# Optimization experiments

Hardware: AMD Instinct MI355X
Metric: run time of the kernel (lower is better)

The kernel has to match this reference:

```python
import jax, jax.numpy as jnp
import numpy as np

EPS = 1e-08

def setup_inputs() -> dict:
    key = jax.random.key(0)
    ks = jax.random.split(key, 5)
    B, T, D, L = 8, 4096, 1024, 24
    data = jax.random.normal(ks[0], (B, T, D), dtype=jnp.float32)
    W_enc = jax.random.normal(ks[1], (L, D), dtype=jnp.float32) * (1.0 / np.sqrt(D))
    b_enc = jax.random.normal(ks[2], (L,), dtype=jnp.float32) * 0.01
    W_dec = jax.random.normal(ks[3], (D, L), dtype=jnp.float32) * (1.0 / np.sqrt(L))
    b_dec = jax.random.normal(ks[4], (D,), dtype=jnp.float32) * 0.01
    ecs = jnp.array([0.1], dtype=jnp.float32)  # error_correction_strength
    ep = jnp.array([1.0], dtype=jnp.float32)   # energy_preservation
    return {"data": data, "W_enc": W_enc, "b_enc": b_enc,
            "W_dec": W_dec, "b_dec": b_dec,
            "error_correction_strength": ecs, "energy_preservation": ep}

def _l2(x):
    return jnp.linalg.norm(x, axis=-1, keepdims=True)

def reference(data, W_enc, b_enc, W_dec, b_dec, error_correction_strength, energy_preservation):
    ecs = error_correction_strength[0]
    ep = energy_preservation[0]
    # --- encode_to_lattice ---
    in_e = _l2(data)                                   # [B,T,1]
    proj = jnp.einsum('btd,ld->btl', data, W_enc) + b_enc
    lattice_points = jnp.round(proj / ecs) * ecs       # quantize to lattice grid
    out_e = _l2(lattice_points)
    lattice = lattice_points * (in_e / (out_e + EPS)) * ep
    # --- decode_from_lattice ---
    in_e2 = _l2(lattice)
    corrected = jnp.where(jnp.abs(lattice) > ecs, lattice, 0.0)
    res = jnp.einsum('btl,dl->btd', corrected, W_dec) + b_dec
    out_e2 = _l2(res)
    return res * (in_e2 / (out_e2 + EPS)) * ep
```

## Files before the change

kernel.cpp:

```cpp
#include <hip/hip_runtime.h>
#include <math.h>

#define EPS 1e-8f

typedef float vfloat4 __attribute__((ext_vector_type(4)));

__global__ void prep_all(const float* __restrict__ W_enc,
                         const float* __restrict__ Wd, const float* __restrict__ bd,
                         float* __restrict__ wt, float* __restrict__ G,
                         float* __restrict__ h, float* __restrict__ bb) {
    int b = blockIdx.x;
    int lane = threadIdx.x;
    if (b < 384) {
        int i = b * 64 + lane;
        int k = i / 24, l = i - k * 24;
        wt[i] = W_enc[l * 1024 + k];
        return;
    }
    b -= 384;
    float s = 0.f;
    if (b < 576) {
        int l = b / 24, m = b - (b / 24) * 24;
        for (int d = lane; d < 1024; d += 64) s = fmaf(Wd[d * 24 + l], Wd[d * 24 + m], s);
    } else if (b < 600) {
        int l = b - 576;
        for (int d = lane; d < 1024; d += 64) s = fmaf(Wd[d * 24 + l], bd[d], s);
    } else {
        for (int d = lane; d < 1024; d += 64) s = fmaf(bd[d], bd[d], s);
    }
    for (int off = 32; off; off >>= 1) s += __shfl_down(s, off);
    if (lane == 0) {
        if (b < 576) G[b] = s;
        else if (b < 600) h[b - 576] = s;
        else *bb = s;
    }
}


constexpr int LD_TILE = 32;
constexpr int TILE_F  = 64 * LD_TILE;
constexpr int NW      = 8;
constexpr int SMEM_F  = NW * TILE_F;

__global__ __launch_bounds__(512, 4)
void leech_main(const float* __restrict__ data,
                const float* __restrict__ b_enc,
                const float* __restrict__ Wd,
                const float* __restrict__ b_dec,
                const float* __restrict__ ecs_p,
                const float* __restrict__ ep_p,
                const float* __restrict__ wt,
                const float* __restrict__ G,
                const float* __restrict__ h,
                const float* __restrict__ bbp,
                float* __restrict__ out)
{
    __shared__ float smem[SMEM_F];
    const int tid = threadIdx.x;
    const int w = tid >> 6;
    const int r = tid & 63;
    const int rowbase = blockIdx.x * 64;

    float* tile = smem + w * TILE_F;

    const int lrow = r >> 3;
    const int lk   = (r & 7) * 4;

    float proj[24];
#pragma unroll
    for (int l = 0; l < 24; ++l) proj[l] = 0.f;
    float ssq = 0.f;

    const int kw = __builtin_amdgcn_readfirstlane((tid >> 6) * 128);

    float4 buf[8];
#pragma unroll
    for (int it = 0; it < 8; ++it)
        buf[it] = *reinterpret_cast<const float4*>(
            data + (size_t)(rowbase + it * 8 + lrow) * 1024 + kw + lk);

    for (int sc = 0; sc < 4; ++sc) {
#pragma unroll
        for (int it = 0; it < 8; ++it) {
            const int row = it * 8 + lrow;
            const int rb = row & 31;
            float* t = tile + row * LD_TILE;
            t[(lk + 0) ^ rb] = buf[it].x;
            t[(lk + 1) ^ rb] = buf[it].y;
            t[(lk + 2) ^ rb] = buf[it].z;
            t[(lk + 3) ^ rb] = buf[it].w;
        }
        if (sc < 3) {
            const int k0n = kw + (sc + 1) * 32;
#pragma unroll
            for (int it = 0; it < 8; ++it)
                buf[it] = *reinterpret_cast<const float4*>(
                    data + (size_t)(rowbase + it * 8 + lrow) * 1024 + k0n + lk);
        }
        const float* xrow = tile + r * LD_TILE;
        const int rb = r & 31;
        const int kofs = __builtin_amdgcn_readfirstlane(kw + sc * 32);
#pragma unroll 8
        for (int kk = 0; kk < 32; ++kk) {
            const float x = xrow[kk ^ rb];
            ssq = fmaf(x, x, ssq);
            const float* wp = wt + (size_t)(kofs + kk) * 24;
#pragma unroll
            for (int l = 0; l < 24; ++l)
                proj[l] = fmaf(wp[l], x, proj[l]);
        }
    }

#pragma unroll
    for (int l = 0; l < 24; ++l)
        smem[w * TILE_F + l * 64 + r] = proj[l];
    smem[w * TILE_F + 24 * 64 + r] = ssq;
    __syncthreads();

    float p[24];
#pragma unroll
    for (int l = 0; l < 24; ++l) {
        float s0 = smem[0 * TILE_F + l * 64 + r] + smem[1 * TILE_F + l * 64 + r];
        float s1 = smem[2 * TILE_F + l * 64 + r] + smem[3 * TILE_F + l * 64 + r];
        float s2 = smem[4 * TILE_F + l * 64 + r] + smem[5 * TILE_F + l * 64 + r];
        float s3 = smem[6 * TILE_F + l * 64 + r] + smem[7 * TILE_F + l * 64 + r];
        p[l] = (s0 + s1) + (s2 + s3);
    }
    float ss;
    {
        float s0 = smem[0 * TILE_F + 24 * 64 + r] + smem[1 * TILE_F + 24 * 64 + r];
        float s1 = smem[2 * TILE_F + 24 * 64 + r] + smem[3 * TILE_F + 24 * 64 + r];
        float s2 = smem[4 * TILE_F + 24 * 64 + r] + smem[5 * TILE_F + 24 * 64 + r];
        float s3 = smem[6 * TILE_F + 24 * 64 + r] + smem[7 * TILE_F + 24 * 64 + r];
        ss = (s0 + s1) + (s2 + s3);
    }
    __syncthreads();

    const float ecs = ecs_p[0];
    const float ep  = ep_p[0];
    const float in_e = sqrtf(ss);

    float lp[24]; float oe = 0.f;
#pragma unroll
    for (int l = 0; l < 24; ++l) {
        const float pp = p[l] + b_enc[l];
        const float q = rintf(pp / ecs) * ecs;
        lp[l] = q;
        oe = fmaf(q, q, oe);
    }
    const float s1 = in_e / (sqrtf(oe) + EPS) * ep;

    float c[24]; float ie = 0.f;
#pragma unroll
    for (int l = 0; l < 24; ++l) {
        const float lat = lp[l] * s1;
        ie = fmaf(lat, lat, ie);
        c[l] = (fabsf(lat) > ecs) ? lat : 0.f;
    }
    const float in_e2 = sqrtf(ie);

    float qacc = bbp[0];
#pragma unroll
    for (int l = 0; l < 24; ++l) {
        float s = 2.f * h[l];
#pragma unroll
        for (int m = 0; m < 24; ++m)
            s = fmaf(G[l * 24 + m], c[m], s);
        qacc = fmaf(s, c[l], qacc);
    }
    const float out_e2 = sqrtf(fmaxf(qacc, 0.f));
    const float s2 = in_e2 / (out_e2 + EPS) * ep;

    for (int sc = 0; sc < 4; ++sc) {
        const int d0 = __builtin_amdgcn_readfirstlane(kw + sc * 32);
        float* trow = tile + r * LD_TILE;
        const int rb = r & 31;
#pragma unroll 4
        for (int dd = 0; dd < 32; ++dd) {
            const int d = d0 + dd;
            const float* wr = Wd + d * 24;
            float acc = b_dec[d];
#pragma unroll
            for (int l = 0; l < 24; ++l)
                acc = fmaf(wr[l], c[l], acc);
            trow[dd ^ rb] = acc * s2;
        }
#pragma unroll
        for (int it = 0; it < 8; ++it) {
            const int row = it * 8 + lrow;
            const int rb2 = row & 31;
            const float* t = tile + row * LD_TILE;
            vfloat4 v;
            v.x = t[(lk + 0) ^ rb2];
            v.y = t[(lk + 1) ^ rb2];
            v.z = t[(lk + 2) ^ rb2];
            v.w = t[(lk + 3) ^ rb2];
            __builtin_nontemporal_store(v, reinterpret_cast<vfloat4*>(
                out + (size_t)(rowbase + row) * 1024 + d0 + lk));
        }
    }
}


extern "C" void kernel_launch(void* const* d_in, const int* in_sizes, int n_in,
                              void* d_out, int out_size, void* d_ws, size_t ws_size,
                              hipStream_t stream) {
    const float* data  = (const float*)d_in[0];
    const float* W_enc = (const float*)d_in[1];
    const float* b_enc = (const float*)d_in[2];
    const float* W_dec = (const float*)d_in[3];
    const float* b_dec = (const float*)d_in[4];
    const float* ecs   = (const float*)d_in[5];
    const float* ep    = (const float*)d_in[6];
    float* out = (float*)d_out;

    float* ws = (float*)d_ws;
    float* wt = ws;
    float* G  = ws + 24576;
    float* h  = ws + 25152;
    float* bb = ws + 25176;

    const int rows = in_sizes[0] / 1024;

    hipLaunchKernelGGL(prep_all, dim3(985), dim3(64), 0, stream,
                       W_enc, W_dec, b_dec, wt, G, h, bb);
    hipLaunchKernelGGL(leech_main, dim3(rows / 64), dim3(512), 0, stream,
                       data, b_enc, W_dec, b_dec, ecs, ep, wt, G, h, bb, out);
}
```

Baseline: 312.4 us.

## Process two rows per thread to reuse weight loads across 128-row blocks

Each block now handles 128 rows instead of 64, with every thread computing the projection, normalisation and decode for two rows. Each weight value loaded from W_enc (transposed) and W_dec is reused for two FMAs, halving weight load traffic per row. The cost is double the register arrays and shared memory (128 KB per block), with launch bounds dropped to 2 blocks per CU and half as many blocks, so occupancy and latency hiding fall.

After: 312.6 us. Within noise of the previous version (+0.1%).

```diff
diff --git a/kernel.cpp b/kernel.cpp
--- a/kernel.cpp
+++ b/kernel.cpp
@@ -37,12 +37,13 @@
 }
 
 
+constexpr int BROWS   = 128;
 constexpr int LD_TILE = 32;
-constexpr int TILE_F  = 64 * LD_TILE;
+constexpr int TILE_F  = BROWS * LD_TILE;
 constexpr int NW      = 8;
 constexpr int SMEM_F  = NW * TILE_F;
 
-__global__ __launch_bounds__(512, 4)
+__global__ __launch_bounds__(512, 2)
 void leech_main(const float* __restrict__ data,
                 const float* __restrict__ b_enc,
                 const float* __restrict__ Wd,
@@ -59,142 +60,199 @@
     const int tid = threadIdx.x;
     const int w = tid >> 6;
     const int r = tid & 63;
-    const int rowbase = blockIdx.x * 64;
+    const int rowbase = blockIdx.x * BROWS;
 
     float* tile = smem + w * TILE_F;
 
     const int lrow = r >> 3;
     const int lk   = (r & 7) * 4;
-
-    float proj[24];
-#pragma unroll
-    for (int l = 0; l < 24; ++l) proj[l] = 0.f;
-    float ssq = 0.f;
+    const int rb   = r & 31;
+
+    float proj0[24], proj1[24];
+#pragma unroll
+    for (int l = 0; l < 24; ++l) { proj0[l] = 0.f; proj1[l] = 0.f; }
+    float ssq0 = 0.f, ssq1 = 0.f;
 
     const int kw = __builtin_amdgcn_readfirstlane((tid >> 6) * 128);
 
-    float4 buf[8];
-#pragma unroll
-    for (int it = 0; it < 8; ++it)
+    float4 buf[16];
+#pragma unroll
+    for (int it = 0; it < 16; ++it)
         buf[it] = *reinterpret_cast<const float4*>(
             data + (size_t)(rowbase + it * 8 + lrow) * 1024 + kw + lk);
 
     for (int sc = 0; sc < 4; ++sc) {
 #pragma unroll
-        for (int it = 0; it < 8; ++it) {
+        for (int it = 0; it < 16; ++it) {
             const int row = it * 8 + lrow;
-            const int rb = row & 31;
+            const int rbw = row & 31;
             float* t = tile + row * LD_TILE;
-            t[(lk + 0) ^ rb] = buf[it].x;
-            t[(lk + 1) ^ rb] = buf[it].y;
-            t[(lk + 2) ^ rb] = buf[it].z;
-            t[(lk + 3) ^ rb] = buf[it].w;
+            t[(lk + 0) ^ rbw] = buf[it].x;
+            t[(lk + 1) ^ rbw] = buf[it].y;
+            t[(lk + 2) ^ rbw] = buf[it].z;
+            t[(lk + 3) ^ rbw] = buf[it].w;
         }
         if (sc < 3) {
             const int k0n = kw + (sc + 1) * 32;
 #pragma unroll
-            for (int it = 0; it < 8; ++it)
+            for (int it = 0; it < 16; ++it)
                 buf[it] = *reinterpret_cast<const float4*>(
                     data + (size_t)(rowbase + it * 8 + lrow) * 1024 + k0n + lk);
         }
-        const float* xrow = tile + r * LD_TILE;
-        const int rb = r & 31;
+        const float* x0 = tile + r * LD_TILE;
+        const float* x1 = tile + (r + 64) * LD_TILE;
         const int kofs = __builtin_amdgcn_readfirstlane(kw + sc * 32);
-#pragma unroll 8
+#pragma unroll 4
         for (int kk = 0; kk < 32; ++kk) {
-            const float x = xrow[kk ^ rb];
-            ssq = fmaf(x, x, ssq);
+            const float a = x0[kk ^ rb];
+            const float b = x1[kk ^ rb];
+            ssq0 = fmaf(a, a, ssq0);
+            ssq1 = fmaf(b, b, ssq1);
             const float* wp = wt + (size_t)(kofs + kk) * 24;
 #pragma unroll
-            for (int l = 0; l < 24; ++l)
-                proj[l] = fmaf(wp[l], x, proj[l]);
-        }
-    }
-
-#pragma unroll
-    for (int l = 0; l < 24; ++l)
-        smem[w * TILE_F + l * 64 + r] = proj[l];
-    smem[w * TILE_F + 24 * 64 + r] = ssq;
+            for (int l = 0; l < 24; ++l) {
+                const float wv = wp[l];
+                proj0[l] = fmaf(wv, a, proj0[l]);
+                proj1[l] = fmaf(wv, b, proj1[l]);
+            }
+        }
+    }
+
+#pragma unroll
+    for (int l = 0; l < 24; ++l) {
+        smem[w * TILE_F + l * 64 + r]        = proj0[l];
+        smem[w * TILE_F + (24 + l) * 64 + r] = proj1[l];
+    }
+    smem[w * TILE_F + 48 * 64 + r] = ssq0;
+    smem[w * TILE_F + 49 * 64 + r] = ssq1;
     __syncthreads();
 
-    float p[24];
+    float p0[24], p1[24];
 #pragma unroll
     for (int l = 0; l < 24; ++l) {
-        float s0 = smem[0 * TILE_F + l * 64 + r] + smem[1 * TILE_F + l * 64 + r];
-        float s1 = smem[2 * TILE_F + l * 64 + r] + smem[3 * TILE_F + l * 64 + r];
-        float s2 = smem[4 * TILE_F + l * 64 + r] + smem[5 * TILE_F + l * 64 + r];
-        float s3 = smem[6 * TILE_F + l * 64 + r] + smem[7 * TILE_F + l * 64 + r];
-        p[l] = (s0 + s1) + (s2 + s3);
-    }
-    float ss;
+        float a0 = smem[0 * TILE_F + l * 64 + r] + smem[1 * TILE_F + l * 64 + r];
+        float a1 = smem[2 * TILE_F + l * 64 + r] + smem[3 * TILE_F + l * 64 + r];
+        float a2 = smem[4 * TILE_F + l * 64 + r] + smem[5 * TILE_F + l * 64 + r];
+        float a3 = smem[6 * TILE_F + l * 64 + r] + smem[7 * TILE_F + l * 64 + r];
+        p0[l] = (a0 + a1) + (a2 + a3);
+        float b0 = smem[0 * TILE_F + (24 + l) * 64 + r] + smem[1 * TILE_F + (24 + l) * 64 + r];
+        float b1 = smem[2 * TILE_F + (24 + l) * 64 + r] + smem[3 * TILE_F + (24 + l) * 64 + r];
+        float b2 = smem[4 * TILE_F + (24 + l) * 64 + r] + smem[5 * TILE_F + (24 + l) * 64 + r];
+        float b3 = smem[6 * TILE_F + (24 + l) * 64 + r] + smem[7 * TILE_F + (24 + l) * 64 + r];
+        p1[l] = (b0 + b1) + (b2 + b3);
+    }
+    float ss0, ss1;
     {
-        float s0 = smem[0 * TILE_F + 24 * 64 + r] + smem[1 * TILE_F + 24 * 64 + r];
-        float s1 = smem[2 * TILE_F + 24 * 64 + r] + smem[3 * TILE_F + 24 * 64 + r];
-        float s2 = smem[4 * TILE_F + 24 * 64 + r] + smem[5 * TILE_F + 24 * 64 + r];
-        float s3 = smem[6 * TILE_F + 24 * 64 + r] + smem[7 * TILE_F + 24 * 64 + r];
-        ss = (s0 + s1) + (s2 + s3);
+        float a0 = smem[0 * TILE_F + 48 * 64 + r] + smem[1 * TILE_F + 48 * 64 + r];
+        float a1 = smem[2 * TILE_F + 48 * 64 + r] + smem[3 * TILE_F + 48 * 64 + r];
+        float a2 = smem[4 * TILE_F + 48 * 64 + r] + smem[5 * TILE_F + 48 * 64 + r];
+        float a3 = smem[6 * TILE_F + 48 * 64 + r] + smem[7 * TILE_F + 48 * 64 + r];
+        ss0 = (a0 + a1) + (a2 + a3);
+        float b0 = smem[0 * TILE_F + 49 * 64 + r] + smem[1 * TILE_F + 49 * 64 + r];
+        float b1 = smem[2 * TILE_F + 49 * 64 + r] + smem[3 * TILE_F + 49 * 64 + r];
+        float b2 = smem[4 * TILE_F + 49 * 64 + r] + smem[5 * TILE_F + 49 * 64 + r];
+        float b3 = smem[6 * TILE_F + 49 * 64 + r] + smem[7 * TILE_F + 49 * 64 + r];
+        ss1 = (b0 + b1) + (b2 + b3);
     }
     __syncthreads();
 
     const float ecs = ecs_p[0];
     const float ep  = ep_p[0];
-    const float in_e = sqrtf(ss);
-
-    float lp[24]; float oe = 0.f;
-#pragma unroll
-    for (int l = 0; l < 24; ++l) {
-        const float pp = p[l] + b_enc[l];
-        const float q = rintf(pp / ecs) * ecs;
-        lp[l] = q;
-        oe = fmaf(q, q, oe);
-    }
-    const float s1 = in_e / (sqrtf(oe) + EPS) * ep;
-
-    float c[24]; float ie = 0.f;
-#pragma unroll
-    for (int l = 0; l < 24; ++l) {
-        const float lat = lp[l] * s1;
-        ie = fmaf(lat, lat, ie);
-        c[l] = (fabsf(lat) > ecs) ? lat : 0.f;
-    }
-    const float in_e2 = sqrtf(ie);
-
-    float qacc = bbp[0];
-#pragma unroll
-    for (int l = 0; l < 24; ++l) {
-        float s = 2.f * h[l];
-#pragma unroll
-        for (int m = 0; m < 24; ++m)
-            s = fmaf(G[l * 24 + m], c[m], s);
-        qacc = fmaf(s, c[l], qacc);
-    }
-    const float out_e2 = sqrtf(fmaxf(qacc, 0.f));
-    const float s2 = in_e2 / (out_e2 + EPS) * ep;
+
+    float c0[24], c1[24];
+    float s2a, s2b;
+    {
+        const float in_e = sqrtf(ss0);
+        float lp[24]; float oe = 0.f;
+#pragma unroll
+        for (int l = 0; l < 24; ++l) {
+            const float pp = p0[l] + b_enc[l];
+            const float q = rintf(pp / ecs) * ecs;
+            lp[l] = q;
+            oe = fmaf(q, q, oe);
+        }
+        const float s1 = in_e / (sqrtf(oe) + EPS) * ep;
+        float ie = 0.f;
+#pragma unroll
+        for (int l = 0; l < 24; ++l) {
+            const float lat = lp[l] * s1;
+            ie = fmaf(lat, lat, ie);
+            c0[l] = (fabsf(lat) > ecs) ? lat : 0.f;
+        }
+        const float in_e2 = sqrtf(ie);
+        float qacc = bbp[0];
+#pragma unroll
+        for (int l = 0; l < 24; ++l) {
+            float s = 2.f * h[l];
+#pragma unroll
+            for (int m = 0; m < 24; ++m)
+                s = fmaf(G[l * 24 + m], c0[m], s);
+            qacc = fmaf(s, c0[l], qacc);
+        }
+        const float out_e2 = sqrtf(fmaxf(qacc, 0.f));
+        s2a = in_e2 / (out_e2 + EPS) * ep;
+    }
+    {
+        const float in_e = sqrtf(ss1);
+        float lp[24]; float oe = 0.f;
+#pragma unroll
+        for (int l = 0; l < 24; ++l) {
+            const float pp = p1[l] + b_enc[l];
+            const float q = rintf(pp / ecs) * ecs;
+            lp[l] = q;
+            oe = fmaf(q, q, oe);
+        }
+        const float s1 = in_e / (sqrtf(oe) + EPS) * ep;
+        float ie = 0.f;
+#pragma unroll
+        for (int l = 0; l < 24; ++l) {
+            const float lat = lp[l] * s1;
+            ie = fmaf(lat, lat, ie);
+            c1[l] = (fabsf(lat) > ecs) ? lat : 0.f;
+        }
+        const float in_e2 = sqrtf(ie);
+        float qacc = bbp[0];
+#pragma unroll
+        for (int l = 0; l < 24; ++l) {
+            float s = 2.f * h[l];
+#pragma unroll
+            for (int m = 0; m < 24; ++m)
+                s = fmaf(G[l * 24 + m], c1[m], s);
+            qacc = fmaf(s, c1[l], qacc);
+        }
+        const float out_e2 = sqrtf(fmaxf(qacc, 0.f));
+        s2b = in_e2 / (out_e2 + EPS) * ep;
+    }
 
     for (int sc = 0; sc < 4; ++sc) {
         const int d0 = __builtin_amdgcn_readfirstlane(kw + sc * 32);
-        float* trow = tile + r * LD_TILE;
-        const int rb = r & 31;
+        float* t0 = tile + r * LD_TILE;
+        float* t1 = tile + (r + 64) * LD_TILE;
 #pragma unroll 4
         for (int dd = 0; dd < 32; ++dd) {
             const int d = d0 + dd;
             const float* wr = Wd + d * 24;
-            float acc = b_dec[d];
-#pragma unroll
-            for (int l = 0; l < 24; ++l)
-                acc = fmaf(wr[l], c[l], acc);
-            trow[dd ^ rb] = acc * s2;
-        }
-#pragma unroll
-        for (int it = 0; it < 8; ++it) {
+            const float bv = b_dec[d];
+            float acc0 = bv, acc1 = bv;
+#pragma unroll
+            for (int l = 0; l < 24; ++l) {
+                const float wv = wr[l];
+                acc0 = fmaf(wv, c0[l], acc0);
+                acc1 = fmaf(wv, c1[l], acc1);
+            }
+            t0[dd ^ rb] = acc0 * s2a;
+            t1[dd ^ rb] = acc1 * s2b;
+        }
+#pragma unroll
+        for (int it = 0; it < 16; ++it) {
             const int row = it * 8 + lrow;
-            const int rb2 = row & 31;
+            const int rbw = row & 31;
             const float* t = tile + row * LD_TILE;
             vfloat4 v;
-            v.x = t[(lk + 0) ^ rb2];
-            v.y = t[(lk + 1) ^ rb2];
-            v.z = t[(lk + 2) ^ rb2];
-            v.w = t[(lk + 3) ^ rb2];
+            v.x = t[(lk + 0) ^ rbw];
+            v.y = t[(lk + 1) ^ rbw];
+            v.z = t[(lk + 2) ^ rbw];
+            v.w = t[(lk + 3) ^ rbw];
             __builtin_nontemporal_store(v, reinterpret_cast<vfloat4*>(
                 out + (size_t)(rowbase + row) * 1024 + d0 + lk));
         }
@@ -224,6 +282,6 @@
 
     hipLaunchKernelGGL(prep_all, dim3(985), dim3(64), 0, stream,
                        W_enc, W_dec, b_dec, wt, G, h, bb);
-    hipLaunchKernelGGL(leech_main, dim3(rows / 64), dim3(512), 0, stream,
+    hipLaunchKernelGGL(leech_main, dim3(rows / BROWS), dim3(512), 0, stream,
                        data, b_enc, W_dec, b_dec, ecs, ep, wt, G, h, bb, out);
 }
```
